# Kernel optimization log

Measured on AMD Instinct MI355X. Metric: run time of the kernel, lower is better.

## Reference

```python
import jax, jax.numpy as jnp
import numpy as np

N, D_IN, D_HID, D_OUT, ORDER = 8192, 512, 1024, 64, 3

def setup_inputs() -> dict:
    key = jax.random.key(0)
    k = jax.random.split(key, 5)
    x = jax.random.normal(k[0], (N, D_IN), dtype=jnp.float32)
    adj = jax.random.uniform(k[1], (ORDER, N, N), dtype=jnp.float32)
    W1 = jax.random.normal(k[2], (ORDER, D_IN, D_HID), dtype=jnp.float32) * (1.0 / np.sqrt(D_IN))
    b1 = jnp.zeros((D_HID,), dtype=jnp.float32)
    W2 = jax.random.normal(k[3], (ORDER, D_HID, D_OUT), dtype=jnp.float32) * (1.0 / np.sqrt(D_HID))
    b2 = jnp.zeros((D_OUT,), dtype=jnp.float32)
    return {"x": x, "preprocessed": adj, "W1": W1, "b1": b1, "W2": W2, "b2": b2}

def multi_val_gc(x, adj, W, b):
    # x: [N, in], adj: [order, N, N], W: [order, in, out]
    xw = jnp.einsum('ni,kio->kno', x, W)          # [order, N, out]
    out = jnp.einsum('knm,kmo->no', adj, xw)      # sum over orders
    return out + b

def reference(x, preprocessed, W1, b1, W2, b2):
    h = multi_val_gc(x, preprocessed, W1, b1)
    h = jax.nn.relu(h)
    # dropout is identity in eval mode
    h = multi_val_gc(h, preprocessed, W2, b2)
    return jax.nn.log_softmax(h, axis=1)
```

## Files before the change

kernel.cpp:

```cpp
#include <hip/hip_runtime.h>
#include <hip/hip_bf16.h>
#include <cstdint>
#include <cstddef>


typedef __bf16 bf16_t;
typedef __bf16 bf16x8 __attribute__((ext_vector_type(8)));
typedef __bf16 bf16x4 __attribute__((ext_vector_type(4)));
typedef float  f32x4  __attribute__((ext_vector_type(4)));

#define NROWS 8192
#define DIN   512
#define DHID  1024
#define DOUT  64
#define ORD   3
#define KTOT  24576

#define GLDS(g, l) __builtin_amdgcn_global_load_lds( \
    (__attribute__((address_space(1))) void*)(g),    \
    (__attribute__((address_space(3))) void*)(l), 16, 0, 0)


__global__ void k_cvt_x(const float* __restrict__ x, bf16_t* __restrict__ xb) {
  int i = blockIdx.x * blockDim.x + threadIdx.x;
  const float4* p = reinterpret_cast<const float4*>(x) + (size_t)i * 2;
  float4 v0 = p[0], v1 = p[1];
  bf16x8 o;
  o[0]=(bf16_t)v0.x; o[1]=(bf16_t)v0.y; o[2]=(bf16_t)v0.z; o[3]=(bf16_t)v0.w;
  o[4]=(bf16_t)v1.x; o[5]=(bf16_t)v1.y; o[6]=(bf16_t)v1.z; o[7]=(bf16_t)v1.w;
  *reinterpret_cast<bf16x8*>(xb + (size_t)i * 8) = o;
}

__global__ void k_cvt_adj(const float* __restrict__ a, bf16_t* __restrict__ ab) {
  size_t i = (size_t)blockIdx.x * blockDim.x + threadIdx.x;
  const size_t stride = (size_t)gridDim.x * blockDim.x;
  const float4* src = reinterpret_cast<const float4*>(a);
#pragma unroll 4
  for (int it = 0; it < 48; ++it, i += stride) {
    float4 v0 = src[i * 2], v1 = src[i * 2 + 1];
    bf16x8 o;
    o[0]=(bf16_t)v0.x; o[1]=(bf16_t)v0.y; o[2]=(bf16_t)v0.z; o[3]=(bf16_t)v0.w;
    o[4]=(bf16_t)v1.x; o[5]=(bf16_t)v1.y; o[6]=(bf16_t)v1.z; o[7]=(bf16_t)v1.w;
    *reinterpret_cast<bf16x8*>(ab + i * 8) = o;
  }
}

__global__ void k_transpose_cvt(const float* __restrict__ src, bf16_t* __restrict__ dst,
                                int R, int C) {
  __shared__ float tile[64][65];
  int ord = blockIdx.z;
  src += (size_t)ord * R * C;
  dst += (size_t)ord * R * C;
  int c0 = blockIdx.x * 64, r0 = blockIdx.y * 64;
  for (int i = 0; i < 16; ++i) {
    int idx = i * 256 + threadIdx.x;
    int r = idx >> 6, c = idx & 63;
    tile[r][c] = src[(size_t)(r0 + r) * C + c0 + c];
  }
  __syncthreads();
  for (int i = 0; i < 16; ++i) {
    int idx = i * 256 + threadIdx.x;
    int cc = idx >> 6, rr = idx & 63;
    dst[(size_t)(c0 + cc) * R + r0 + rr] = (bf16_t)tile[rr][cc];
  }
}

__global__ __launch_bounds__(256) void k_gemm_xw1(
    const bf16_t* __restrict__ xb,
    const bf16_t* __restrict__ w1t,
    bf16_t* __restrict__ xw1t)
{
  __shared__ bf16_t As[128 * 64];
  __shared__ bf16_t Bs[128 * 64];
  int ntile = blockIdx.x, mtile = blockIdx.y, ord = blockIdx.z;
  int tid = threadIdx.x, lane = tid & 63, wid = tid >> 6;
  int wm = wid >> 1, wn = wid & 1;
  int sl = (lane & 7) ^ (lane >> 3);
  f32x4 acc[4][4] = {};
  const bf16_t* w1o = w1t + (size_t)ord * DHID * DIN;
  for (int kt = 0; kt < DIN; kt += 64) {
    for (int j = 0; j < 4; ++j) {
      int q = wid * 4 + j;
      int row = q * 8 + (lane >> 3);
      GLDS(xb + (size_t)(mtile * 128 + row) * DIN + kt + sl * 8, &As[q * 512]);
    }
    for (int j = 0; j < 4; ++j) {
      int q = wid * 4 + j;
      int row = q * 8 + (lane >> 3);
      GLDS(w1o + (size_t)(ntile * 128 + row) * DIN + kt + sl * 8, &Bs[q * 512]);
    }
    __syncthreads();
    for (int ks = 0; ks < 2; ++ks) {
      int psl = ((ks << 2) + (lane >> 4)) ^ (lane & 7);
      bf16x8 a[4], b[4];
      for (int f = 0; f < 4; ++f)
        a[f] = *reinterpret_cast<const bf16x8*>(&As[(wm * 64 + f * 16 + (lane & 15)) * 64 + psl * 8]);
      for (int f = 0; f < 4; ++f)
        b[f] = *reinterpret_cast<const bf16x8*>(&Bs[(wn * 64 + f * 16 + (lane & 15)) * 64 + psl * 8]);
      for (int fm = 0; fm < 4; ++fm)
        for (int fn = 0; fn < 4; ++fn)
          acc[fm][fn] = __builtin_amdgcn_mfma_f32_16x16x32_bf16(a[fm], b[fn], acc[fm][fn], 0, 0, 0);
    }
    __syncthreads();
  }
  for (int fm = 0; fm < 4; ++fm)
    for (int fn = 0; fn < 4; ++fn) {
      int o  = ntile * 128 + wn * 64 + fn * 16 + (lane & 15);
      int n0 = mtile * 128 + wm * 64 + fm * 16 + ((lane >> 4) << 2);
      bf16x4 v;
      v[0] = (bf16_t)acc[fm][fn][0]; v[1] = (bf16_t)acc[fm][fn][1];
      v[2] = (bf16_t)acc[fm][fn][2]; v[3] = (bf16_t)acc[fm][fn][3];
      *reinterpret_cast<bf16x4*>(&xw1t[(size_t)o * KTOT + ord * NROWS + n0]) = v;
    }
}

__global__ __launch_bounds__(256) void k_gemm_h(
    const bf16_t* __restrict__ adjb,
    const bf16_t* __restrict__ xw1t,
    const float* __restrict__ b1,
    bf16_t* __restrict__ h)
{
  __shared__ bf16_t As[128 * 64];
  __shared__ bf16_t Bs[128 * 64];
  int d = blockIdx.x;
  int xcd = d & 7;
  int idx = d >> 3;
  int mtile = xcd * 8 + (idx >> 3);
  int ntile = idx & 7;
  int tid = threadIdx.x, lane = tid & 63, wid = tid >> 6;
  int wm = wid >> 1, wn = wid & 1;
  int sl = (lane & 7) ^ (lane >> 3);
  const size_t NN = (size_t)NROWS * NROWS;
  f32x4 acc[4][4] = {};
  for (int kt = 0; kt < KTOT / 64; ++kt) {
    int kk = kt * 64;
    int ord = kk >> 13, mcol = kk & 8191;
    const bf16_t* ao = adjb + (size_t)ord * NN + (size_t)(mtile * 128) * NROWS + mcol;
    for (int j = 0; j < 4; ++j) {
      int q = wid * 4 + j;
      int row = q * 8 + (lane >> 3);
      GLDS(ao + (size_t)row * NROWS + sl * 8, &As[q * 512]);
    }
    for (int j = 0; j < 4; ++j) {
      int q = wid * 4 + j;
      int row = q * 8 + (lane >> 3);
      GLDS(xw1t + (size_t)(ntile * 128 + row) * KTOT + kk + sl * 8, &Bs[q * 512]);
    }
    __syncthreads();
    for (int ks = 0; ks < 2; ++ks) {
      int psl = ((ks << 2) + (lane >> 4)) ^ (lane & 7);
      bf16x8 a[4], b[4];
      for (int f = 0; f < 4; ++f)
        a[f] = *reinterpret_cast<const bf16x8*>(&As[(wm * 64 + f * 16 + (lane & 15)) * 64 + psl * 8]);
      for (int f = 0; f < 4; ++f)
        b[f] = *reinterpret_cast<const bf16x8*>(&Bs[(wn * 64 + f * 16 + (lane & 15)) * 64 + psl * 8]);
      for (int fm = 0; fm < 4; ++fm)
        for (int fn = 0; fn < 4; ++fn)
          acc[fm][fn] = __builtin_amdgcn_mfma_f32_16x16x32_bf16(a[fm], b[fn], acc[fm][fn], 0, 0, 0);
    }
    __syncthreads();
  }
  for (int fm = 0; fm < 4; ++fm)
    for (int fn = 0; fn < 4; ++fn) {
      int o  = ntile * 128 + wn * 64 + fn * 16 + (lane & 15);
      float bias = b1[o];
      int n0 = mtile * 128 + wm * 64 + fm * 16 + ((lane >> 4) << 2);
      for (int j = 0; j < 4; ++j) {
        float v = acc[fm][fn][j] + bias;
        v = v > 0.0f ? v : 0.0f;
        h[(size_t)(n0 + j) * DHID + o] = (bf16_t)v;
      }
    }
}

__global__ __launch_bounds__(256) void k_gemm_xw2(
    const bf16_t* __restrict__ h,
    const bf16_t* __restrict__ w2t,
    bf16_t* __restrict__ xw2t)
{
  __shared__ bf16_t As[128 * 64];
  __shared__ bf16_t Bs[64 * 64];
  int mtile = blockIdx.x, ord = blockIdx.y;
  int tid = threadIdx.x, lane = tid & 63, wid = tid >> 6;
  int wm = wid >> 1, wn = wid & 1;
  int sl = (lane & 7) ^ (lane >> 3);
  f32x4 acc[4][2] = {};
  const bf16_t* w2o = w2t + (size_t)ord * DOUT * DHID;
  for (int kt = 0; kt < DHID; kt += 64) {
    for (int j = 0; j < 4; ++j) {
      int q = wid * 4 + j;
      int row = q * 8 + (lane >> 3);
      GLDS(h + (size_t)(mtile * 128 + row) * DHID + kt + sl * 8, &As[q * 512]);
    }
    for (int j = 0; j < 2; ++j) {
      int q = wid * 2 + j;
      int row = q * 8 + (lane >> 3);
      GLDS(w2o + (size_t)row * DHID + kt + sl * 8, &Bs[q * 512]);
    }
    __syncthreads();
    for (int ks = 0; ks < 2; ++ks) {
      int psl = ((ks << 2) + (lane >> 4)) ^ (lane & 7);
      bf16x8 a[4], b[2];
      for (int f = 0; f < 4; ++f)
        a[f] = *reinterpret_cast<const bf16x8*>(&As[(wm * 64 + f * 16 + (lane & 15)) * 64 + psl * 8]);
      for (int f = 0; f < 2; ++f)
        b[f] = *reinterpret_cast<const bf16x8*>(&Bs[(wn * 32 + f * 16 + (lane & 15)) * 64 + psl * 8]);
      for (int fm = 0; fm < 4; ++fm)
        for (int fn = 0; fn < 2; ++fn)
          acc[fm][fn] = __builtin_amdgcn_mfma_f32_16x16x32_bf16(a[fm], b[fn], acc[fm][fn], 0, 0, 0);
    }
    __syncthreads();
  }
  for (int fm = 0; fm < 4; ++fm)
    for (int fn = 0; fn < 2; ++fn) {
      int o2 = wn * 32 + fn * 16 + (lane & 15);
      int n0 = mtile * 128 + wm * 64 + fm * 16 + ((lane >> 4) << 2);
      bf16x4 v;
      v[0] = (bf16_t)acc[fm][fn][0]; v[1] = (bf16_t)acc[fm][fn][1];
      v[2] = (bf16_t)acc[fm][fn][2]; v[3] = (bf16_t)acc[fm][fn][3];
      *reinterpret_cast<bf16x4*>(&xw2t[(size_t)o2 * KTOT + ord * NROWS + n0]) = v;
    }
}

__global__ __launch_bounds__(256) void k_gemm_out(
    const bf16_t* __restrict__ adjb,
    const bf16_t* __restrict__ xw2t,
    float* __restrict__ part)
{
  __shared__ bf16_t As[128 * 64];
  __shared__ bf16_t Bs[64 * 64];
  int mtile = blockIdx.x, ksp = blockIdx.y;
  int tid = threadIdx.x, lane = tid & 63, wid = tid >> 6;
  int wm = wid >> 1, wn = wid & 1;
  int sl = (lane & 7) ^ (lane >> 3);
  const size_t NN = (size_t)NROWS * NROWS;
  f32x4 acc[4][2] = {};
  for (int kt = ksp * 48; kt < ksp * 48 + 48; ++kt) {
    int kk = kt * 64;
    int ord = kk >> 13, mcol = kk & 8191;
    const bf16_t* ao = adjb + (size_t)ord * NN + (size_t)(mtile * 128) * NROWS + mcol;
    for (int j = 0; j < 4; ++j) {
      int q = wid * 4 + j;
      int row = q * 8 + (lane >> 3);
      GLDS(ao + (size_t)row * NROWS + sl * 8, &As[q * 512]);
    }
    for (int j = 0; j < 2; ++j) {
      int q = wid * 2 + j;
      int row = q * 8 + (lane >> 3);
      GLDS(xw2t + (size_t)row * KTOT + kk + sl * 8, &Bs[q * 512]);
    }
    __syncthreads();
    for (int ks = 0; ks < 2; ++ks) {
      int psl = ((ks << 2) + (lane >> 4)) ^ (lane & 7);
      bf16x8 a[4], b[2];
      for (int f = 0; f < 4; ++f)
        a[f] = *reinterpret_cast<const bf16x8*>(&As[(wm * 64 + f * 16 + (lane & 15)) * 64 + psl * 8]);
      for (int f = 0; f < 2; ++f)
        b[f] = *reinterpret_cast<const bf16x8*>(&Bs[(wn * 32 + f * 16 + (lane & 15)) * 64 + psl * 8]);
      for (int fm = 0; fm < 4; ++fm)
        for (int fn = 0; fn < 2; ++fn)
          acc[fm][fn] = __builtin_amdgcn_mfma_f32_16x16x32_bf16(a[fm], b[fn], acc[fm][fn], 0, 0, 0);
    }
    __syncthreads();
  }
  float* pout = part + (size_t)ksp * NROWS * DOUT;
  for (int fm = 0; fm < 4; ++fm)
    for (int fn = 0; fn < 2; ++fn) {
      int o2 = wn * 32 + fn * 16 + (lane & 15);
      int n0 = mtile * 128 + wm * 64 + fm * 16 + ((lane >> 4) << 2);
      for (int j = 0; j < 4; ++j)
        pout[(size_t)(n0 + j) * DOUT + o2] = acc[fm][fn][j];
    }
}

__global__ __launch_bounds__(256) void k_gemm_h_f32(
    const float* __restrict__ adj, const bf16_t* __restrict__ xw1t,
    const float* __restrict__ b1, bf16_t* __restrict__ h)
{
  __shared__ bf16_t As[128 * 64];
  __shared__ bf16_t Bs[128 * 64];
  int d = blockIdx.x;
  int xcd = d & 7, idx = d >> 3;
  int mtile = xcd * 8 + (idx >> 3), ntile = idx & 7;
  int tid = threadIdx.x, lane = tid & 63, wid = tid >> 6;
  int wm = wid >> 1, wn = wid & 1;
  int sl = (lane & 7) ^ (lane >> 3);
  f32x4 acc[4][4] = {};
  for (int kt = 0; kt < KTOT / 64; ++kt) {
    int kk0 = kt * 64;
    int ord = kk0 >> 13, mcol = kk0 & 8191;
    for (int j = 0; j < 4; ++j) {
      int q = wid * 4 + j;
      int row = q * 8 + (lane >> 3);
      GLDS(xw1t + (size_t)(ntile * 128 + row) * KTOT + kk0 + sl * 8, &Bs[q * 512]);
    }
    const float* abase = adj + (size_t)ord * NROWS * NROWS + (size_t)(mtile * 128) * NROWS + mcol;
    bf16x8 st[4]; int mrow[4], kb[4];
    for (int i = 0; i < 4; ++i) {
      int c = i * 256 + tid;
      mrow[i] = c >> 3; kb[i] = c & 7;
      const float4* p = reinterpret_cast<const float4*>(abase + (size_t)mrow[i] * NROWS + kb[i] * 8);
      float4 v0 = p[0], v1 = p[1];
      bf16x8 o;
      o[0]=(bf16_t)v0.x; o[1]=(bf16_t)v0.y; o[2]=(bf16_t)v0.z; o[3]=(bf16_t)v0.w;
      o[4]=(bf16_t)v1.x; o[5]=(bf16_t)v1.y; o[6]=(bf16_t)v1.z; o[7]=(bf16_t)v1.w;
      st[i] = o;
    }
    for (int i = 0; i < 4; ++i)
      *reinterpret_cast<bf16x8*>(&As[mrow[i] * 64 + (kb[i] ^ (mrow[i] & 7)) * 8]) = st[i];
    __syncthreads();
    for (int ks = 0; ks < 2; ++ks) {
      int psl = ((ks << 2) + (lane >> 4)) ^ (lane & 7);
      bf16x8 a[4], b[4];
      for (int f = 0; f < 4; ++f)
        a[f] = *reinterpret_cast<const bf16x8*>(&As[(wm * 64 + f * 16 + (lane & 15)) * 64 + psl * 8]);
      for (int f = 0; f < 4; ++f)
        b[f] = *reinterpret_cast<const bf16x8*>(&Bs[(wn * 64 + f * 16 + (lane & 15)) * 64 + psl * 8]);
      for (int fm = 0; fm < 4; ++fm)
        for (int fn = 0; fn < 4; ++fn)
          acc[fm][fn] = __builtin_amdgcn_mfma_f32_16x16x32_bf16(a[fm], b[fn], acc[fm][fn], 0, 0, 0);
    }
    __syncthreads();
  }
  for (int fm = 0; fm < 4; ++fm)
    for (int fn = 0; fn < 4; ++fn) {
      int o  = ntile * 128 + wn * 64 + fn * 16 + (lane & 15);
      float bias = b1[o];
      int n0 = mtile * 128 + wm * 64 + fm * 16 + ((lane >> 4) << 2);
      for (int j = 0; j < 4; ++j) {
        float v = acc[fm][fn][j] + bias;
        v = v > 0.0f ? v : 0.0f;
        h[(size_t)(n0 + j) * DHID + o] = (bf16_t)v;
      }
    }
}

__global__ __launch_bounds__(256) void k_gemm_out_f32(
    const float* __restrict__ adj, const bf16_t* __restrict__ xw2t,
    float* __restrict__ part)
{
  __shared__ bf16_t As[128 * 64];
  __shared__ bf16_t Bs[64 * 64];
  int mtile = blockIdx.x, ksp = blockIdx.y;
  int tid = threadIdx.x, lane = tid & 63, wid = tid >> 6;
  int wm = wid >> 1, wn = wid & 1;
  int sl = (lane & 7) ^ (lane >> 3);
  f32x4 acc[4][2] = {};
  for (int kt = ksp * 48; kt < ksp * 48 + 48; ++kt) {
    int kk0 = kt * 64;
    int ord = kk0 >> 13, mcol = kk0 & 8191;
    for (int j = 0; j < 2; ++j) {
      int q = wid * 2 + j;
      int row = q * 8 + (lane >> 3);
      GLDS(xw2t + (size_t)row * KTOT + kk0 + sl * 8, &Bs[q * 512]);
    }
    const float* abase = adj + (size_t)ord * NROWS * NROWS + (size_t)(mtile * 128) * NROWS + mcol;
    bf16x8 st[4]; int mrow[4], kb[4];
    for (int i = 0; i < 4; ++i) {
      int c = i * 256 + tid;
      mrow[i] = c >> 3; kb[i] = c & 7;
      const float4* p = reinterpret_cast<const float4*>(abase + (size_t)mrow[i] * NROWS + kb[i] * 8);
      float4 v0 = p[0], v1 = p[1];
      bf16x8 o;
      o[0]=(bf16_t)v0.x; o[1]=(bf16_t)v0.y; o[2]=(bf16_t)v0.z; o[3]=(bf16_t)v0.w;
      o[4]=(bf16_t)v1.x; o[5]=(bf16_t)v1.y; o[6]=(bf16_t)v1.z; o[7]=(bf16_t)v1.w;
      st[i] = o;
    }
    for (int i = 0; i < 4; ++i)
      *reinterpret_cast<bf16x8*>(&As[mrow[i] * 64 + (kb[i] ^ (mrow[i] & 7)) * 8]) = st[i];
    __syncthreads();
    for (int ks = 0; ks < 2; ++ks) {
      int psl = ((ks << 2) + (lane >> 4)) ^ (lane & 7);
      bf16x8 a[4], b[2];
      for (int f = 0; f < 4; ++f)
        a[f] = *reinterpret_cast<const bf16x8*>(&As[(wm * 64 + f * 16 + (lane & 15)) * 64 + psl * 8]);
      for (int f = 0; f < 2; ++f)
        b[f] = *reinterpret_cast<const bf16x8*>(&Bs[(wn * 32 + f * 16 + (lane & 15)) * 64 + psl * 8]);
      for (int fm = 0; fm < 4; ++fm)
        for (int fn = 0; fn < 2; ++fn)
          acc[fm][fn] = __builtin_amdgcn_mfma_f32_16x16x32_bf16(a[fm], b[fn], acc[fm][fn], 0, 0, 0);
    }
    __syncthreads();
  }
  float* pout = part + (size_t)ksp * NROWS * DOUT;
  for (int fm = 0; fm < 4; ++fm)
    for (int fn = 0; fn < 2; ++fn) {
      int o2 = wn * 32 + fn * 16 + (lane & 15);
      int n0 = mtile * 128 + wm * 64 + fm * 16 + ((lane >> 4) << 2);
      for (int j = 0; j < 4; ++j)
        pout[(size_t)(n0 + j) * DOUT + o2] = acc[fm][fn][j];
    }
}

__global__ void k_logsoftmax(const float* __restrict__ part, const float* __restrict__ b2,
                             float* __restrict__ out) {
  int wid = threadIdx.x >> 6, lane = threadIdx.x & 63;
  int n = blockIdx.x * 4 + wid;
  size_t s = (size_t)NROWS * DOUT;
  float v = b2[lane];
#pragma unroll
  for (int p = 0; p < 8; ++p)
    v += part[(size_t)p * s + (size_t)n * DOUT + lane];
  float mx = v;
  for (int d = 32; d; d >>= 1) mx = fmaxf(mx, __shfl_xor(mx, d));
  float e = expf(v - mx);
  float sum = e;
  for (int d = 32; d; d >>= 1) sum += __shfl_xor(sum, d);
  out[(size_t)n * DOUT + lane] = (v - mx) - logf(sum);
}

extern "C" void kernel_launch(void* const* d_in, const int* in_sizes, int n_in,
                              void* d_out, int out_size, void* d_ws, size_t ws_size,
                              hipStream_t stream) {
  const float* x   = (const float*)d_in[0];
  const float* adj = (const float*)d_in[1];
  const float* W1  = (const float*)d_in[2];
  const float* b1  = (const float*)d_in[3];
  const float* W2  = (const float*)d_in[4];
  const float* b2  = (const float*)d_in[5];
  float* out = (float*)d_out;
  char* ws = (char*)d_ws;

  const size_t ADJB_SZ = 402653184ULL;
  const size_t NEED    = 484835328ULL;

  if (ws_size >= NEED) {
    bf16_t* adjb = (bf16_t*)(ws + 0);
    bf16_t* xb   = (bf16_t*)(ws + ADJB_SZ);
    bf16_t* w1t  = (bf16_t*)(ws + ADJB_SZ + 8388608);
    bf16_t* w2t  = (bf16_t*)(ws + ADJB_SZ + 11534336);
    bf16_t* xw1t = (bf16_t*)(ws + ADJB_SZ + 11927552);
    bf16_t* h    = (bf16_t*)(ws + ADJB_SZ + 62259200);
    bf16_t* xw2t = (bf16_t*)(ws + ADJB_SZ + 79036416);
    float*  part = (float*)(ws + ADJB_SZ + 11927552);

    k_cvt_adj<<<2048, 256, 0, stream>>>(adj, adjb);
    k_cvt_x<<<2048, 256, 0, stream>>>(x, xb);
    k_transpose_cvt<<<dim3(16, 8, 3), 256, 0, stream>>>(W1, w1t, DIN, DHID);
    k_transpose_cvt<<<dim3(1, 16, 3), 256, 0, stream>>>(W2, w2t, DHID, DOUT);
    k_gemm_xw1<<<dim3(8, 64, 3), 256, 0, stream>>>(xb, w1t, xw1t);
    k_gemm_h<<<512, 256, 0, stream>>>(adjb, xw1t, b1, h);
    k_gemm_xw2<<<dim3(64, 3), 256, 0, stream>>>(h, w2t, xw2t);
    k_gemm_out<<<dim3(64, 8), 256, 0, stream>>>(adjb, xw2t, part);
    k_logsoftmax<<<2048, 256, 0, stream>>>(part, b2, out);
  } else {
    bf16_t* xb   = (bf16_t*)(ws + 0);
    bf16_t* w1t  = (bf16_t*)(ws + 8388608);
    bf16_t* w2t  = (bf16_t*)(ws + 11534336);
    bf16_t* xw1t = (bf16_t*)(ws + 11927552);
    bf16_t* h    = (bf16_t*)(ws + 62259200);
    bf16_t* xw2t = (bf16_t*)(ws + 79036416);
    float*  part = (float*)(ws + 11927552);

    k_cvt_x<<<2048, 256, 0, stream>>>(x, xb);
    k_transpose_cvt<<<dim3(16, 8, 3), 256, 0, stream>>>(W1, w1t, DIN, DHID);
    k_transpose_cvt<<<dim3(1, 16, 3), 256, 0, stream>>>(W2, w2t, DHID, DOUT);
    k_gemm_xw1<<<dim3(8, 64, 3), 256, 0, stream>>>(xb, w1t, xw1t);
    k_gemm_h_f32<<<512, 256, 0, stream>>>(adj, xw1t, b1, h);
    k_gemm_xw2<<<dim3(64, 3), 256, 0, stream>>>(h, w2t, xw2t);
    k_gemm_out_f32<<<dim3(64, 8), 256, 0, stream>>>(adj, xw2t, part);
    k_logsoftmax<<<2048, 256, 0, stream>>>(part, b2, out);
  }
}
```

Before: 942.4 us.

## Double-buffer LDS tiles in adjacency GEMMs to overlap loads with MFMA

Converts k_gemm_h and k_gemm_out to a two-stage LDS ping-pong. The next K-tile's global_load_lds is issued before computing on the current tile, and one barrier per iteration replaces two. This aims to hide global memory latency behind MFMA work in the bandwidth-heavy adjacency GEMMs. It doubles LDS use per block, which can lower occupancy. The log-softmax kernel is only relocated in the file.

```diff
diff --git a/kernel.cpp b/kernel.cpp
--- a/kernel.cpp
+++ b/kernel.cpp
@@ -120,8 +120,8 @@
     const float* __restrict__ b1,
     bf16_t* __restrict__ h)
 {
-  __shared__ bf16_t As[128 * 64];
-  __shared__ bf16_t Bs[128 * 64];
+  __shared__ bf16_t As[2][128 * 64];
+  __shared__ bf16_t Bs[2][128 * 64];
   int d = blockIdx.x;
   int xcd = d & 7;
   int idx = d >> 3;
@@ -132,34 +132,48 @@
   int sl = (lane & 7) ^ (lane >> 3);
   const size_t NN = (size_t)NROWS * NROWS;
   f32x4 acc[4][4] = {};
-  for (int kt = 0; kt < KTOT / 64; ++kt) {
+
+  auto stage = [&](int buf, int kt) {
     int kk = kt * 64;
     int ord = kk >> 13, mcol = kk & 8191;
     const bf16_t* ao = adjb + (size_t)ord * NN + (size_t)(mtile * 128) * NROWS + mcol;
-    for (int j = 0; j < 4; ++j) {
-      int q = wid * 4 + j;
-      int row = q * 8 + (lane >> 3);
-      GLDS(ao + (size_t)row * NROWS + sl * 8, &As[q * 512]);
-    }
-    for (int j = 0; j < 4; ++j) {
-      int q = wid * 4 + j;
-      int row = q * 8 + (lane >> 3);
-      GLDS(xw1t + (size_t)(ntile * 128 + row) * KTOT + kk + sl * 8, &Bs[q * 512]);
-    }
-    __syncthreads();
+#pragma unroll
+    for (int j = 0; j < 4; ++j) {
+      int q = wid * 4 + j;
+      int row = q * 8 + (lane >> 3);
+      GLDS(ao + (size_t)row * NROWS + sl * 8, &As[buf][q * 512]);
+    }
+#pragma unroll
+    for (int j = 0; j < 4; ++j) {
+      int q = wid * 4 + j;
+      int row = q * 8 + (lane >> 3);
+      GLDS(xw1t + (size_t)(ntile * 128 + row) * KTOT + kk + sl * 8, &Bs[buf][q * 512]);
+    }
+  };
+
+  stage(0, 0);
+  __syncthreads();
+
+  for (int kt = 0; kt < KTOT / 64; ++kt) {
+    int cur = kt & 1;
+    if (kt + 1 < KTOT / 64) stage(cur ^ 1, kt + 1);
+    const bf16_t* Ac = &As[cur][0];
+    const bf16_t* Bc = &Bs[cur][0];
+#pragma unroll
     for (int ks = 0; ks < 2; ++ks) {
       int psl = ((ks << 2) + (lane >> 4)) ^ (lane & 7);
       bf16x8 a[4], b[4];
       for (int f = 0; f < 4; ++f)
-        a[f] = *reinterpret_cast<const bf16x8*>(&As[(wm * 64 + f * 16 + (lane & 15)) * 64 + psl * 8]);
-      for (int f = 0; f < 4; ++f)
-        b[f] = *reinterpret_cast<const bf16x8*>(&Bs[(wn * 64 + f * 16 + (lane & 15)) * 64 + psl * 8]);
+        a[f] = *reinterpret_cast<const bf16x8*>(&Ac[(wm * 64 + f * 16 + (lane & 15)) * 64 + psl * 8]);
+      for (int f = 0; f < 4; ++f)
+        b[f] = *reinterpret_cast<const bf16x8*>(&Bc[(wn * 64 + f * 16 + (lane & 15)) * 64 + psl * 8]);
       for (int fm = 0; fm < 4; ++fm)
         for (int fn = 0; fn < 4; ++fn)
           acc[fm][fn] = __builtin_amdgcn_mfma_f32_16x16x32_bf16(a[fm], b[fn], acc[fm][fn], 0, 0, 0);
     }
     __syncthreads();
   }
+
   for (int fm = 0; fm < 4; ++fm)
     for (int fn = 0; fn < 4; ++fn) {
       int o  = ntile * 128 + wn * 64 + fn * 16 + (lane & 15);
@@ -227,42 +241,57 @@
     const bf16_t* __restrict__ xw2t,
     float* __restrict__ part)
 {
-  __shared__ bf16_t As[128 * 64];
-  __shared__ bf16_t Bs[64 * 64];
+  __shared__ bf16_t As[2][128 * 64];
+  __shared__ bf16_t Bs[2][64 * 64];
   int mtile = blockIdx.x, ksp = blockIdx.y;
   int tid = threadIdx.x, lane = tid & 63, wid = tid >> 6;
   int wm = wid >> 1, wn = wid & 1;
   int sl = (lane & 7) ^ (lane >> 3);
   const size_t NN = (size_t)NROWS * NROWS;
   f32x4 acc[4][2] = {};
-  for (int kt = ksp * 48; kt < ksp * 48 + 48; ++kt) {
-    int kk = kt * 64;
+  const int T0 = ksp * 48, NT = 48;
+
+  auto stage = [&](int buf, int t) {
+    int kk = (T0 + t) * 64;
     int ord = kk >> 13, mcol = kk & 8191;
     const bf16_t* ao = adjb + (size_t)ord * NN + (size_t)(mtile * 128) * NROWS + mcol;
-    for (int j = 0; j < 4; ++j) {
-      int q = wid * 4 + j;
-      int row = q * 8 + (lane >> 3);
-      GLDS(ao + (size_t)row * NROWS + sl * 8, &As[q * 512]);
-    }
+#pragma unroll
+    for (int j = 0; j < 4; ++j) {
+      int q = wid * 4 + j;
+      int row = q * 8 + (lane >> 3);
+      GLDS(ao + (size_t)row * NROWS + sl * 8, &As[buf][q * 512]);
+    }
+#pragma unroll
     for (int j = 0; j < 2; ++j) {
       int q = wid * 2 + j;
       int row = q * 8 + (lane >> 3);
-      GLDS(xw2t + (size_t)row * KTOT + kk + sl * 8, &Bs[q * 512]);
-    }
-    __syncthreads();
+      GLDS(xw2t + (size_t)row * KTOT + kk + sl * 8, &Bs[buf][q * 512]);
+    }
+  };
+
+  stage(0, 0);
+  __syncthreads();
+
+  for (int t = 0; t < NT; ++t) {
+    int cur = t & 1;
+    if (t + 1 < NT) stage(cur ^ 1, t + 1);
+    const bf16_t* Ac = &As[cur][0];
+    const bf16_t* Bc = &Bs[cur][0];
+#pragma unroll
     for (int ks = 0; ks < 2; ++ks) {
       int psl = ((ks << 2) + (lane >> 4)) ^ (lane & 7);
       bf16x8 a[4], b[2];
       for (int f = 0; f < 4; ++f)
-        a[f] = *reinterpret_cast<const bf16x8*>(&As[(wm * 64 + f * 16 + (lane & 15)) * 64 + psl * 8]);
+        a[f] = *reinterpret_cast<const bf16x8*>(&Ac[(wm * 64 + f * 16 + (lane & 15)) * 64 + psl * 8]);
       for (int f = 0; f < 2; ++f)
-        b[f] = *reinterpret_cast<const bf16x8*>(&Bs[(wn * 32 + f * 16 + (lane & 15)) * 64 + psl * 8]);
+        b[f] = *reinterpret_cast<const bf16x8*>(&Bc[(wn * 32 + f * 16 + (lane & 15)) * 64 + psl * 8]);
       for (int fm = 0; fm < 4; ++fm)
         for (int fn = 0; fn < 2; ++fn)
           acc[fm][fn] = __builtin_amdgcn_mfma_f32_16x16x32_bf16(a[fm], b[fn], acc[fm][fn], 0, 0, 0);
     }
     __syncthreads();
   }
+
   float* pout = part + (size_t)ksp * NROWS * DOUT;
   for (int fm = 0; fm < 4; ++fm)
     for (int fn = 0; fn < 2; ++fn) {
@@ -271,6 +300,23 @@
       for (int j = 0; j < 4; ++j)
         pout[(size_t)(n0 + j) * DOUT + o2] = acc[fm][fn][j];
     }
+}
+
+__global__ void k_logsoftmax(const float* __restrict__ part, const float* __restrict__ b2,
+                             float* __restrict__ out) {
+  int wid = threadIdx.x >> 6, lane = threadIdx.x & 63;
+  int n = blockIdx.x * 4 + wid;
+  size_t s = (size_t)NROWS * DOUT;
+  float v = b2[lane];
+#pragma unroll
+  for (int p = 0; p < 8; ++p)
+    v += part[(size_t)p * s + (size_t)n * DOUT + lane];
+  float mx = v;
+  for (int d = 32; d; d >>= 1) mx = fmaxf(mx, __shfl_xor(mx, d));
+  float e = expf(v - mx);
+  float sum = e;
+  for (int d = 32; d; d >>= 1) sum += __shfl_xor(sum, d);
+  out[(size_t)n * DOUT + lane] = (v - mx) - logf(sum);
 }
 
 __global__ __launch_bounds__(256) void k_gemm_h_f32(
@@ -390,23 +436,6 @@
       for (int j = 0; j < 4; ++j)
         pout[(size_t)(n0 + j) * DOUT + o2] = acc[fm][fn][j];
     }
-}
-
-__global__ void k_logsoftmax(const float* __restrict__ part, const float* __restrict__ b2,
-                             float* __restrict__ out) {
-  int wid = threadIdx.x >> 6, lane = threadIdx.x & 63;
-  int n = blockIdx.x * 4 + wid;
-  size_t s = (size_t)NROWS * DOUT;
-  float v = b2[lane];
-#pragma unroll
-  for (int p = 0; p < 8; ++p)
-    v += part[(size_t)p * s + (size_t)n * DOUT + lane];
-  float mx = v;
-  for (int d = 32; d; d >>= 1) mx = fmaxf(mx, __shfl_xor(mx, d));
-  float e = expf(v - mx);
-  float sum = e;
-  for (int d = 32; d; d >>= 1) sum += __shfl_xor(sum, d);
-  out[(size_t)n * DOUT + lane] = (v - mx) - logf(sum);
 }
 
 extern "C" void kernel_launch(void* const* d_in, const int* in_sizes, int n_in,
```

After: 949.2 us. Within noise of the previous version (+0.7%).
